# Kernel tuning notes

Hardware: AMD Instinct MI355X
Metric: run time of the kernel (lower is better)

The kernel has to match this reference:

```python
import jax, jax.numpy as jnp
import numpy as np

L = 4          # num_layers
D = 64         # embedding_dim
N = 100000     # nodes
E = 1250000    # edges
B = 2048       # graphs (batch.max()+1, fixed for jit)
ATOM_V = 128   # atom feature vocab per field
BOND_V = 8     # bond feature vocab per field
BN_EPS = 1e-5


def setup_inputs() -> dict:
    key = jax.random.key(0)
    ks = jax.random.split(key, 10)
    x_feat = jax.random.randint(ks[0], (N, 9), 0, 119)
    edge_index = jax.random.randint(ks[1], (2, E), 0, N)
    edge_attr = jax.random.randint(ks[2], (E, 3), 0, 5)
    batch = jnp.sort(jax.random.randint(ks[3], (N,), 0, B))
    s = 0.02
    atom_emb = jax.random.normal(ks[4], (9, ATOM_V, D), jnp.float32) * s
    bond_emb = jax.random.normal(ks[5], (L, 3, BOND_V, D), jnp.float32) * s
    eps = jnp.zeros((L,), jnp.float32)
    W1 = jax.random.normal(ks[6], (L, D, 2 * D), jnp.float32) / np.sqrt(D).astype(np.float32)
    b1 = jnp.zeros((L, 2 * D), jnp.float32)
    bn1_g = jnp.ones((L, 2 * D), jnp.float32)
    bn1_b = jnp.zeros((L, 2 * D), jnp.float32)
    W2 = jax.random.normal(ks[7], (L, 2 * D, D), jnp.float32) / np.sqrt(2 * D).astype(np.float32)
    b2 = jnp.zeros((L, D), jnp.float32)
    bn2_g = jnp.ones((L, D), jnp.float32)
    bn2_b = jnp.zeros((L, D), jnp.float32)
    return dict(atom_emb=atom_emb, bond_emb=bond_emb, eps=eps,
                W1=W1, b1=b1, bn1_g=bn1_g, bn1_b=bn1_b,
                W2=W2, b2=b2, bn2_g=bn2_g, bn2_b=bn2_b,
                x_feat=x_feat, edge_index=edge_index, edge_attr=edge_attr, batch=batch)


def _bn(h, g, b):
    # training-mode BatchNorm1d over node dim (biased variance, as torch forward)
    m = h.mean(axis=0)
    v = jnp.mean((h - m) ** 2, axis=0)
    return (h - m) * jax.lax.rsqrt(v + BN_EPS) * g + b


def reference(atom_emb, bond_emb, eps, W1, b1, bn1_g, bn1_b, W2, b2, bn2_g, bn2_b,
              x_feat, edge_index, edge_attr, batch):
    n = x_feat.shape[0]
    # AtomEncoder: sum of per-field embedding lookups -> [N, D]
    h = atom_emb[jnp.arange(9), x_feat].sum(axis=1)
    src, dst = edge_index[0], edge_index[1]
    for l in range(L):
        # BondEncoder for this layer: [E, D]
        e = bond_emb[l][jnp.arange(3), edge_attr].sum(axis=1)
        # message: relu(x_j + edge_emb); aggregate: scatter_add at target nodes
        msg = jax.nn.relu(h[src] + e)
        agg = jax.ops.segment_sum(msg, dst, num_segments=N)
        z = (1.0 + eps[l]) * h + agg
        # MLP: Linear -> BN -> ReLU -> Linear
        z = jax.nn.relu(_bn(z @ W1[l] + b1[l], bn1_g[l], bn1_b[l]))
        z = z @ W2[l] + b2[l]
        # outer per-layer BatchNorm
        h = _bn(z, bn2_g[l], bn2_b[l])
        if l != L - 1:
            h = jax.nn.relu(h)
        # dropout disabled (eval/deterministic reference)
    node_repr = h
    # mean pooling by graph id
    out_feat = jax.ops.segment_sum(h, batch, num_segments=B)
    cnt = jax.ops.segment_sum(jnp.ones((n, 1), h.dtype), batch, num_segments=B)
    graph_repr = out_feat / (cnt + 1e-9)
    return node_repr, graph_repr
```

## Files before the change

kernel.cpp:

```cpp
#include <hip/hip_runtime.h>

#define NN 100000
#define NE 1250000
#define NB 2048
#define NZB 391

typedef __attribute__((ext_vector_type(8))) short short8;
typedef __attribute__((ext_vector_type(4))) float floatx4;

__device__ inline unsigned short f2bf(float f) {
    unsigned u = __float_as_uint(f);
    u = u + 0x7fffu + ((u >> 16) & 1u);
    return (unsigned short)(u >> 16);
}
__device__ inline float bf2f(unsigned short h) {
    return __uint_as_float(((unsigned)h) << 16);
}

__global__ void atom_encode(const float* __restrict__ atom_emb,
                            const int* __restrict__ x_feat,
                            float* __restrict__ h, unsigned short* __restrict__ h16) {
    int id = blockIdx.x * 256 + threadIdx.x;
    int n = id >> 4, q = id & 15;
    floatx4 acc = {0.f, 0.f, 0.f, 0.f};
    for (int f = 0; f < 9; f++) {
        int v = x_feat[n * 9 + f];
        const floatx4* p = (const floatx4*)(atom_emb + (size_t)(f * 128 + v) * 64);
        acc += p[q];
    }
    ((floatx4*)h)[(size_t)n * 16 + q] = acc;
    ushort4 hv;
    hv.x = f2bf(acc[0]); hv.y = f2bf(acc[1]); hv.z = f2bf(acc[2]); hv.w = f2bf(acc[3]);
    ((ushort4*)h16)[(size_t)n * 16 + q] = hv;
}

__global__ void deg_count(const int* __restrict__ ei, int* __restrict__ csr) {
    int e = (blockIdx.x * 256 + threadIdx.x) * 2;
    if (e < NE) {
        int2 d = *(const int2*)(ei + NE + e);
        atomicAdd(&csr[d.x], 1);
        if (e + 1 < NE) atomicAdd(&csr[d.y], 1);
    }
}

__global__ void scan_local(int* __restrict__ csr, int* __restrict__ bsum) {
    __shared__ int ls[256];
    int tid = threadIdx.x;
    int base = blockIdx.x * 1024 + tid * 4;
    int4 v = make_int4(0, 0, 0, 0);
    if (base + 3 < NN) {
        v = *(const int4*)(csr + base);
    } else {
        if (base + 0 < NN) v.x = csr[base + 0];
        if (base + 1 < NN) v.y = csr[base + 1];
        if (base + 2 < NN) v.z = csr[base + 2];
        if (base + 3 < NN) v.w = csr[base + 3];
    }
    int s = v.x + v.y + v.z + v.w;
    ls[tid] = s;
    __syncthreads();
    for (int d = 1; d < 256; d <<= 1) {
        int t = (tid >= d) ? ls[tid - d] : 0;
        __syncthreads();
        ls[tid] += t;
        __syncthreads();
    }
    if (tid == 255) bsum[blockIdx.x] = ls[255];
    int e0 = tid ? ls[tid - 1] : 0;
    int4 w;
    w.x = e0; w.y = e0 + v.x; w.z = w.y + v.y; w.w = w.z + v.z;
    if (base + 3 < NN) {
        *(int4*)(csr + base) = w;
    } else {
        if (base + 0 < NN) csr[base + 0] = w.x;
        if (base + 1 < NN) csr[base + 1] = w.y;
        if (base + 2 < NN) csr[base + 2] = w.z;
        if (base + 3 < NN) csr[base + 3] = w.w;
    }
}

__global__ void scan_add(int* __restrict__ csr, const int* __restrict__ bsum) {
    __shared__ int red[128];
    int tid = threadIdx.x;
    if (tid < 128) {
        red[tid] = (tid < blockIdx.x && tid < 98) ? bsum[tid] : 0;
    }
    __syncthreads();
    for (int d = 64; d > 0; d >>= 1) {
        if (tid < d) red[tid] += red[tid + d];
        __syncthreads();
    }
    int off = red[0];
    int base = blockIdx.x * 1024 + tid * 4;
    if (base + 3 < NN) {
        int4 v = *(const int4*)(csr + base);
        v.x += off; v.y += off; v.z += off; v.w += off;
        *(int4*)(csr + base) = v;
    } else {
        for (int i = 0; i < 4; i++)
            if (base + i < NN) csr[base + i] += off;
    }
}

__global__ void csr_fill(const int* __restrict__ ei, const int* __restrict__ ea,
                         int* __restrict__ csr, unsigned* __restrict__ epack) {
    int e = blockIdx.x * 256 + threadIdx.x;
    if (e >= NE) return;
    int dst = ei[NE + e];
    unsigned at = (unsigned)(ea[e * 3] | (ea[e * 3 + 1] << 3) | (ea[e * 3 + 2] << 6));
    unsigned rec = (unsigned)ei[e] | (at << 17);
    int pos = atomicAdd(&csr[dst], 1);
    epack[pos] = rec;
}

template <bool HASBN>
__global__ void gather_k(const float* __restrict__ x, const unsigned short* __restrict__ x16,
                         const float* __restrict__ bond_emb,
                         const float* __restrict__ eps, const int* __restrict__ csr,
                         const unsigned* __restrict__ epack, int l,
                         const float* __restrict__ stats, const float* __restrict__ bn_g,
                         const float* __restrict__ bn_b, float* __restrict__ agg) {
    __shared__ float be[24 * 64];
    __shared__ float ca[64], cb[64];
    int tid = threadIdx.x;
    const float* bsrc = bond_emb + (size_t)l * 1536;
    for (int i = tid; i < 1536; i += 256) be[i] = bsrc[i];
    if (tid < 64) {
        if (HASBN) {
            float s = 0.f, ss = 0.f;
            for (int j = 0; j < 8; j++) {
                s  += stats[j * 128 + tid];
                ss += stats[j * 128 + 64 + tid];
            }
            float mean = s / NN;
            float var  = ss / NN - mean * mean;
            float a = bn_g[(l - 1) * 64 + tid] * rsqrtf(var + 1e-5f);
            ca[tid] = a;
            cb[tid] = bn_b[(l - 1) * 64 + tid] - mean * a;
        } else {
            ca[tid] = 1.f; cb[tid] = 0.f;
        }
    }
    __syncthreads();
    int id = blockIdx.x * 256 + tid;
    int n = id >> 4, q = id & 15;
    float s = 1.0f + eps[l];
    floatx4 cav = *(const floatx4*)&ca[q * 4];
    floatx4 cbv = *(const floatx4*)&cb[q * 4];
    floatx4 xv = ((const floatx4*)x)[(size_t)n * 16 + q];
    if (HASBN) {
        xv[0] = fmaxf(cav[0] * xv[0] + cbv[0], 0.f);
        xv[1] = fmaxf(cav[1] * xv[1] + cbv[1], 0.f);
        xv[2] = fmaxf(cav[2] * xv[2] + cbv[2], 0.f);
        xv[3] = fmaxf(cav[3] * xv[3] + cbv[3], 0.f);
    }
    floatx4 acc = xv * s;
    floatx4 accB = {0.f, 0.f, 0.f, 0.f};
    int k0 = n ? csr[n - 1] : 0;
    int k1 = csr[n];
    const floatx4* beq = (const floatx4*)be;
    int k = k0;
    for (; k + 1 < k1; k += 2) {
        unsigned r0 = epack[k];
        unsigned r1 = epack[k + 1];
        ushort4 h0 = ((const ushort4*)x16)[(size_t)(r0 & 0x1FFFFu) * 16 + q];
        ushort4 h1 = ((const ushort4*)x16)[(size_t)(r1 & 0x1FFFFu) * 16 + q];
        floatx4 m0 = {bf2f(h0.x), bf2f(h0.y), bf2f(h0.z), bf2f(h0.w)};
        floatx4 m1 = {bf2f(h1.x), bf2f(h1.y), bf2f(h1.z), bf2f(h1.w)};
        if (HASBN) {
            m0[0] = fmaxf(cav[0] * m0[0] + cbv[0], 0.f);
            m0[1] = fmaxf(cav[1] * m0[1] + cbv[1], 0.f);
            m0[2] = fmaxf(cav[2] * m0[2] + cbv[2], 0.f);
            m0[3] = fmaxf(cav[3] * m0[3] + cbv[3], 0.f);
            m1[0] = fmaxf(cav[0] * m1[0] + cbv[0], 0.f);
            m1[1] = fmaxf(cav[1] * m1[1] + cbv[1], 0.f);
            m1[2] = fmaxf(cav[2] * m1[2] + cbv[2], 0.f);
            m1[3] = fmaxf(cav[3] * m1[3] + cbv[3], 0.f);
        }
        m0 += beq[((r0 >> 17) & 7u) * 16 + q];
        m0 += beq[(8 + ((r0 >> 20) & 7u)) * 16 + q];
        m0 += beq[(16 + ((r0 >> 23) & 7u)) * 16 + q];
        m1 += beq[((r1 >> 17) & 7u) * 16 + q];
        m1 += beq[(8 + ((r1 >> 20) & 7u)) * 16 + q];
        m1 += beq[(16 + ((r1 >> 23) & 7u)) * 16 + q];
        acc[0] += fmaxf(m0[0], 0.f);
        acc[1] += fmaxf(m0[1], 0.f);
        acc[2] += fmaxf(m0[2], 0.f);
        acc[3] += fmaxf(m0[3], 0.f);
        accB[0] += fmaxf(m1[0], 0.f);
        accB[1] += fmaxf(m1[1], 0.f);
        accB[2] += fmaxf(m1[2], 0.f);
        accB[3] += fmaxf(m1[3], 0.f);
    }
    if (k < k1) {
        unsigned r0 = epack[k];
        ushort4 h0 = ((const ushort4*)x16)[(size_t)(r0 & 0x1FFFFu) * 16 + q];
        floatx4 m0 = {bf2f(h0.x), bf2f(h0.y), bf2f(h0.z), bf2f(h0.w)};
        if (HASBN) {
            m0[0] = fmaxf(cav[0] * m0[0] + cbv[0], 0.f);
            m0[1] = fmaxf(cav[1] * m0[1] + cbv[1], 0.f);
            m0[2] = fmaxf(cav[2] * m0[2] + cbv[2], 0.f);
            m0[3] = fmaxf(cav[3] * m0[3] + cbv[3], 0.f);
        }
        m0 += beq[((r0 >> 17) & 7u) * 16 + q];
        m0 += beq[(8 + ((r0 >> 20) & 7u)) * 16 + q];
        m0 += beq[(16 + ((r0 >> 23) & 7u)) * 16 + q];
        acc[0] += fmaxf(m0[0], 0.f);
        acc[1] += fmaxf(m0[1], 0.f);
        acc[2] += fmaxf(m0[2], 0.f);
        acc[3] += fmaxf(m0[3], 0.f);
    }
    acc += accB;
    ((floatx4*)agg)[(size_t)n * 16 + q] = acc;
}

__global__ void wcvt(const float* __restrict__ W1, const float* __restrict__ W2,
                     unsigned short* __restrict__ w1h, unsigned short* __restrict__ w2h) {
    int id = blockIdx.x * 256 + threadIdx.x;
    if (id < 32768) {
        int l = id >> 13, rem = id & 8191, c = rem >> 6, k = rem & 63;
        w1h[id] = f2bf(W1[l * 8192 + k * 128 + c]);
    } else {
        int id2 = id - 32768;
        int l = id2 >> 13, rem = id2 & 8191, c = rem >> 7, k = rem & 127;
        w2h[id2] = f2bf(W2[l * 8192 + k * 64 + c]);
    }
}

#define MFMA __builtin_amdgcn_mfma_f32_16x16x32_bf16

#define ZS 264
__launch_bounds__(256)
__global__ void zstat(const float* __restrict__ z, float* __restrict__ Gpart,
                      float* __restrict__ zsum) {
    __shared__ char smem[67584];
    unsigned short* zh = (unsigned short*)smem;
    unsigned short* zl = zh + 64 * ZS;
    int tid = threadIdx.x;
    int c2 = tid & 31;
    int nof = tid >> 5;
    int wv = tid >> 6, lane = tid & 63, m = lane & 15, qd = lane >> 4;
    float2 csum = make_float2(0.f, 0.f);
    floatx4 acc[8];
    for (int t = 0; t < 8; t++) acc[t] = (floatx4){0.f, 0.f, 0.f, 0.f};
    int base = blockIdx.x * 256;
    for (int it = 0; it < 32; it++) {
        int n = it * 8 + nof;
        int node = base + n;
        float2 v = make_float2(0.f, 0.f);
        if (node < NN) v = ((const float2*)z)[(size_t)node * 32 + c2];
        csum.x += v.x; csum.y += v.y;
        unsigned short hx = f2bf(v.x), hy = f2bf(v.y);
        zh[(2 * c2) * ZS + n] = hx;
        zh[(2 * c2 + 1) * ZS + n] = hy;
        zl[(2 * c2) * ZS + n] = f2bf(v.x - bf2f(hx));
        zl[(2 * c2 + 1) * ZS + n] = f2bf(v.y - bf2f(hy));
    }
    __syncthreads();
    for (int kc = 0; kc < 8; kc++) {
        short8 ah = *(const short8*)&zh[(wv * 16 + m) * ZS + kc * 32 + qd * 8];
        for (int j = 0; j < 4; j++) {
            short8 bh = *(const short8*)&zh[(j * 16 + m) * ZS + kc * 32 + qd * 8];
            short8 bl = *(const short8*)&zl[(j * 16 + m) * ZS + kc * 32 + qd * 8];
            acc[j * 2]     = MFMA(ah, bh, acc[j * 2], 0, 0, 0);
            acc[j * 2 + 1] = MFMA(ah, bl, acc[j * 2 + 1], 0, 0, 0);
        }
    }
    float* gp = Gpart + (size_t)blockIdx.x * 8192;
    for (int j = 0; j < 4; j++)
        for (int r = 0; r < 4; r++) {
            int idx = (wv * 16 + qd * 4 + r) * 64 + j * 16 + m;
            gp[idx] = acc[j * 2][r];
            gp[4096 + idx] = acc[j * 2 + 1][r];
        }
    __syncthreads();
    float* red = (float*)smem;
    red[tid] = csum.x; red[256 + tid] = csum.y;
    __syncthreads();
    if (tid < 32) {
        float sx = 0.f, sy = 0.f;
        for (int k = 0; k < 8; k++) { sx += red[k * 32 + tid]; sy += red[256 + k * 32 + tid]; }
        atomicAdd(&zsum[2 * tid], sx);
        atomicAdd(&zsum[2 * tid + 1], sy);
    }
}

__global__ void greduce(const float* __restrict__ Gpart, float* __restrict__ G) {
    int idx = blockIdx.x * 256 + threadIdx.x;
    int b0 = blockIdx.y * 98;
    int b1 = b0 + 98; if (b1 > NZB) b1 = NZB;
    float s = 0.f;
    for (int b = b0; b < b1; b++) s += Gpart[(size_t)b * 8192 + idx];
    atomicAdd(&G[idx], s);
}

__launch_bounds__(256)
__global__ void bn1stat(const float* __restrict__ W1, const float* __restrict__ b1,
                        const float* __restrict__ G, const float* __restrict__ zsum,
                        int l, const float* __restrict__ bn_g, const float* __restrict__ bn_b,
                        float* __restrict__ cab) {
    __shared__ float wc[64];
    __shared__ float red[256];
    int c = blockIdx.x;
    int tid = threadIdx.x;
    if (tid < 64) wc[tid] = bf2f(f2bf(W1[l * 8192 + tid * 128 + c]));
    __syncthreads();
    float q = 0.f;
    for (int p = 0; p < 16; p++) {
        int idx = p * 256 + tid;
        int i = idx >> 6, j = idx & 63;
        q += wc[i] * wc[j] * (G[idx] + 2.f * G[4096 + idx]);
    }
    red[tid] = q;
    __syncthreads();
    for (int d = 128; d > 0; d >>= 1) {
        if (tid < d) red[tid] += red[tid + d];
        __syncthreads();
    }
    if (tid == 0) {
        float s1 = 0.f;
        for (int k = 0; k < 64; k++) s1 += zsum[k] * wc[k];
        float bc = b1[l * 128 + c];
        double mean = ((double)s1 + (double)NN * (double)bc) / (double)NN;
        double ex2  = ((double)red[0] + 2.0 * (double)bc * (double)s1
                       + (double)NN * (double)bc * (double)bc) / (double)NN;
        float var = (float)(ex2 - mean * mean);
        float a = bn_g[l * 128 + c] * rsqrtf(var + 1e-5f);
        cab[c] = a;
        cab[128 + c] = bn_b[l * 128 + c] - (float)mean * a + a * bc;
    }
}

#define RS 140
__launch_bounds__(256, 4)
__global__ void mlp_fused(const float* __restrict__ z,
                          const unsigned short* __restrict__ w1h,
                          const unsigned short* __restrict__ w2h,
                          const float* __restrict__ b2,
                          const float* __restrict__ cab, int l,
                          float* __restrict__ t2, unsigned short* __restrict__ t216,
                          float* __restrict__ s2f) {
    __shared__ unsigned short smem[4 * 2 * 16 * RS];
    int tid = threadIdx.x;
    int wv = tid >> 6, lane = tid & 63, m = lane & 15, qd = lane >> 4;
    int base = blockIdx.x * 64;
    unsigned short* rbh = smem + wv * (2 * 16 * RS);
    unsigned short* rbl = rbh + 16 * RS;

    int row = base + wv * 16 + m;
    floatx4 z0a = {0.f, 0.f, 0.f, 0.f}, z0b = z0a, z1a = z0a, z1b = z0a;
    if (row < NN) {
        const floatx4* zp = (const floatx4*)z + (size_t)row * 16;
        z0a = zp[qd * 2];
        z0b = zp[qd * 2 + 1];
        z1a = zp[8 + qd * 2];
        z1b = zp[8 + qd * 2 + 1];
    }
    short8 ah0, al0, ah1, al1;
    for (int j = 0; j < 4; j++) {
        unsigned short h;
        h = f2bf(z0a[j]); ah0[j] = (short)h; al0[j] = (short)f2bf(z0a[j] - bf2f(h));
        h = f2bf(z0b[j]); ah0[4 + j] = (short)h; al0[4 + j] = (short)f2bf(z0b[j] - bf2f(h));
        h = f2bf(z1a[j]); ah1[j] = (short)h; al1[j] = (short)f2bf(z1a[j] - bf2f(h));
        h = f2bf(z1b[j]); ah1[4 + j] = (short)h; al1[4 + j] = (short)f2bf(z1b[j] - bf2f(h));
    }

    float caT[8], cbT[8];
    #pragma unroll
    for (int t = 0; t < 8; t++) {
        caT[t] = cab[t * 16 + m];
        cbT[t] = cab[128 + t * 16 + m];
    }

    const unsigned short* w1p = w1h + l * 8192;
    floatx4 acc1[8];
    #pragma unroll
    for (int t = 0; t < 8; t++) {
        const unsigned short* wp = w1p + (t * 16 + m) * 64;
        short8 bh0 = *(const short8*)(wp + qd * 8);
        short8 bh1 = *(const short8*)(wp + 32 + qd * 8);
        floatx4 c0 = {0.f, 0.f, 0.f, 0.f};
        c0 = MFMA(ah0, bh0, c0, 0, 0, 0);
        c0 = MFMA(al0, bh0, c0, 0, 0, 0);
        c0 = MFMA(ah1, bh1, c0, 0, 0, 0);
        c0 = MFMA(al1, bh1, c0, 0, 0, 0);
        acc1[t] = c0;
    }

    #pragma unroll
    for (int t = 0; t < 8; t++) {
        float a = caT[t], b = cbT[t];
        #pragma unroll
        for (int r = 0; r < 4; r++) {
            int rl = qd * 4 + r;
            float rv = fmaxf(a * acc1[t][r] + b, 0.f);
            unsigned short hh = f2bf(rv);
            rbh[rl * RS + t * 16 + m] = hh;
            rbl[rl * RS + t * 16 + m] = f2bf(rv - bf2f(hh));
        }
    }
    short8 ahf[4], alf[4];
    #pragma unroll
    for (int kh = 0; kh < 4; kh++) {
        ahf[kh] = *(const short8*)&rbh[m * RS + kh * 32 + qd * 8];
        alf[kh] = *(const short8*)&rbl[m * RS + kh * 32 + qd * 8];
    }

    const unsigned short* w2p = w2h + l * 8192;
    floatx4 acc2[4];
    #pragma unroll
    for (int t = 0; t < 4; t++) {
        const unsigned short* wp = w2p + (t * 16 + m) * 128;
        floatx4 c0 = {0.f, 0.f, 0.f, 0.f};
        #pragma unroll
        for (int kh = 0; kh < 4; kh++) {
            short8 bh = *(const short8*)(wp + kh * 32 + qd * 8);
            c0 = MFMA(ahf[kh], bh, c0, 0, 0, 0);
            c0 = MFMA(alf[kh], bh, c0, 0, 0, 0);
        }
        acc2[t] = c0;
    }

    float* redw = (float*)rbh;
    const float* bias = b2 + l * 64;
    #pragma unroll
    for (int t = 0; t < 4; t++) {
        int col = t * 16 + m;
        float bv = bias[col];
        float s = 0.f, ss = 0.f;
        #pragma unroll
        for (int r = 0; r < 4; r++) {
            int node = base + wv * 16 + qd * 4 + r;
            if (node < NN) {
                float v = acc2[t][r] + bv;
                t2[(size_t)node * 64 + col] = v;
                t216[(size_t)node * 64 + col] = f2bf(v);
                s += v; ss += v * v;
            }
        }
        redw[col * 4 + qd] = s;
        redw[256 + col * 4 + qd] = ss;
    }
    __syncthreads();
    if (tid < 64) {
        float s = 0.f, ss = 0.f;
        for (int w = 0; w < 4; w++) {
            const float* rw = (const float*)(smem + w * (2 * 16 * RS));
            for (int q = 0; q < 4; q++) {
                s  += rw[tid * 4 + q];
                ss += rw[256 + tid * 4 + q];
            }
        }
        float* dst = s2f + (blockIdx.x & 7) * 128;
        atomicAdd(&dst[tid], s);
        atomicAdd(&dst[64 + tid], ss);
    }
}

__global__ void bnapply_last(const float* __restrict__ t2, const float* __restrict__ bn_g,
                             const float* __restrict__ bn_b, const float* __restrict__ s2f,
                             float* __restrict__ out, float* __restrict__ gsum,
                             float* __restrict__ gcnt, const int* __restrict__ batch) {
    __shared__ float ca[64], cb[64];
    int tid = threadIdx.x;
    if (tid < 64) {
        float s = 0.f, ss = 0.f;
        for (int j = 0; j < 8; j++) {
            s  += s2f[j * 128 + tid];
            ss += s2f[j * 128 + 64 + tid];
        }
        float mean = s / NN;
        float var  = ss / NN - mean * mean;
        float a = bn_g[3 * 64 + tid] * rsqrtf(var + 1e-5f);
        ca[tid] = a;
        cb[tid] = bn_b[3 * 64 + tid] - mean * a;
    }
    __syncthreads();
    int c = tid & 63, nsub = tid >> 6;
    int nodebase = blockIdx.x * 64;
    float accv = 0.f, accc = 0.f;
    int curg = -1;
    for (int it = 0; it < 16; it++) {
        int node = nodebase + it * 4 + nsub;
        if (node < NN) {
            float v = ca[c] * t2[(size_t)node * 64 + c] + cb[c];
            out[(size_t)node * 64 + c] = v;
            int g = batch[node];
            if (g != curg) {
                if (curg >= 0) {
                    atomicAdd(&gsum[(size_t)curg * 64 + c], accv);
                    if (c == 0) atomicAdd(&gcnt[curg], accc);
                }
                curg = g; accv = v; accc = 1.f;
            } else {
                accv += v; accc += 1.f;
            }
        }
    }
    if (curg >= 0) {
        atomicAdd(&gsum[(size_t)curg * 64 + c], accv);
        if (c == 0) atomicAdd(&gcnt[curg], accc);
    }
}

__global__ void pool_div(const float* __restrict__ gsum, const float* __restrict__ gcnt,
                         float* __restrict__ out) {
    int id = blockIdx.x * 256 + threadIdx.x;
    int g = id >> 6;
    out[(size_t)NN * 64 + id] = gsum[id] / (gcnt[g] + 1e-9f);
}

extern "C" void kernel_launch(void* const* d_in, const int* in_sizes, int n_in,
                              void* d_out, int out_size, void* d_ws, size_t ws_size,
                              hipStream_t stream) {
    const float* atom_emb = (const float*)d_in[0];
    const float* bond_emb = (const float*)d_in[1];
    const float* eps      = (const float*)d_in[2];
    const float* W1       = (const float*)d_in[3];
    const float* b1       = (const float*)d_in[4];
    const float* bn1_g    = (const float*)d_in[5];
    const float* bn1_b    = (const float*)d_in[6];
    const float* W2       = (const float*)d_in[7];
    const float* b2       = (const float*)d_in[8];
    const float* bn2_g    = (const float*)d_in[9];
    const float* bn2_b    = (const float*)d_in[10];
    const int* x_feat     = (const int*)d_in[11];
    const int* edge_index = (const int*)d_in[12];
    const int* edge_attr  = (const int*)d_in[13];
    const int* batch      = (const int*)d_in[14];
    float* out = (float*)d_out;

    char* ws = (char*)d_ws;
    float* gsum   = (float*)ws;   ws += (size_t)NB * 64 * 4;
    float* gcnt   = (float*)ws;   ws += NB * 4;
    int* csr      = (int*)ws;     ws += (size_t)NN * 4;
    float* zsum   = (float*)ws;   ws += 4 * 64 * 4;
    float* G      = (float*)ws;   ws += (size_t)4 * 8192 * 4;
    float* s2f    = (float*)ws;   ws += (size_t)4 * 8 * 128 * 4;
    size_t zbytes = (size_t)(ws - (char*)d_ws);
    float* cab      = (float*)ws;     ws += 256 * 4;
    int* bsum       = (int*)ws;       ws += 128 * 4;
    unsigned* epack = (unsigned*)ws;  ws += (size_t)NE * 4;
    float* Gpart = (float*)ws;    ws += (size_t)NZB * 8192 * 4;
    float* xbuf = (float*)ws;     ws += (size_t)NN * 64 * 4;
    unsigned short* x16 = (unsigned short*)ws; ws += (size_t)NN * 64 * 2;
    float* agg  = (float*)ws;     ws += (size_t)NN * 64 * 4;
    unsigned short* w1h = (unsigned short*)ws; ws += 32768 * 2;
    unsigned short* w2h = (unsigned short*)ws; ws += 32768 * 2;

    hipMemsetAsync((void*)gsum, 0, zbytes, stream);

    wcvt<<<256, 256, 0, stream>>>(W1, W2, w1h, w2h);
    deg_count<<<2442, 256, 0, stream>>>(edge_index, csr);
    scan_local<<<98, 256, 0, stream>>>(csr, bsum);
    scan_add<<<98, 256, 0, stream>>>(csr, bsum);
    csr_fill<<<4883, 256, 0, stream>>>(edge_index, edge_attr, csr, epack);
    atom_encode<<<6250, 256, 0, stream>>>(atom_emb, x_feat, xbuf, x16);

    for (int l = 0; l < 4; l++) {
        if (l == 0) {
            gather_k<false><<<6250, 256, 0, stream>>>(xbuf, x16, bond_emb, eps, csr, epack, l,
                                                      nullptr, nullptr, nullptr, agg);
        } else {
            gather_k<true><<<6250, 256, 0, stream>>>(xbuf, x16, bond_emb, eps, csr, epack, l,
                                                     s2f + (size_t)(l - 1) * 1024,
                                                     bn2_g, bn2_b, agg);
        }
        float* Gl = G + (size_t)l * 8192;
        zstat<<<NZB, 256, 0, stream>>>(agg, Gpart, zsum + l * 64);
        greduce<<<dim3(32, 4), 256, 0, stream>>>(Gpart, Gl);
        bn1stat<<<128, 256, 0, stream>>>(W1, b1, Gl, zsum + l * 64, l, bn1_g, bn1_b, cab);
        mlp_fused<<<1563, 256, 0, stream>>>(agg, w1h, w2h, b2, cab, l,
                                            xbuf, x16, s2f + (size_t)l * 1024);
    }
    bnapply_last<<<1563, 256, 0, stream>>>(xbuf, bn2_g, bn2_b, s2f + (size_t)3 * 1024,
                                           out, gsum, gcnt, batch);
    pool_div<<<512, 256, 0, stream>>>(gsum, gcnt, out);
}
```

Measured before the change: 890.5 us.

## Shard edges by destination range into per-XCC FIFOs before CSR build

Replaces the direct degree-count and CSR-fill passes with a staging pass that bins edges into 64 FIFOs, keyed by destination shard and block id. Two follow-up passes then drain those FIFOs, preferring queues matched to the XCC they run on. The aim is to keep atomics on csr local to one XCD's L2 and so cut cross-die atomic traffic. In exchange it adds an extra pass that writes and reads about 10 MB, a fixed FIFO capacity (FCAP) that could overflow on skewed inputs, and extra atomics for work stealing.

```diff
diff --git a/kernel.cpp b/kernel.cpp
--- a/kernel.cpp
+++ b/kernel.cpp
@@ -4,6 +4,7 @@
 #define NE 1250000
 #define NB 2048
 #define NZB 391
+#define FCAP 21504
 
 typedef __attribute__((ext_vector_type(8))) short short8;
 typedef __attribute__((ext_vector_type(4))) float floatx4;
@@ -15,6 +16,12 @@
 }
 __device__ inline float bf2f(unsigned short h) {
     return __uint_as_float(((unsigned)h) << 16);
+}
+
+__device__ inline int xcc8() {
+    int x;
+    asm volatile("s_getreg_b32 %0, hwreg(HW_REG_XCC_ID, 0, 32)" : "=s"(x));
+    return x & 7;
 }
 
 __global__ void atom_encode(const float* __restrict__ atom_emb,
@@ -34,12 +41,60 @@
     ((ushort4*)h16)[(size_t)n * 16 + q] = hv;
 }
 
-__global__ void deg_count(const int* __restrict__ ei, int* __restrict__ csr) {
-    int e = (blockIdx.x * 256 + threadIdx.x) * 2;
-    if (e < NE) {
-        int2 d = *(const int2*)(ei + NE + e);
-        atomicAdd(&csr[d.x], 1);
-        if (e + 1 < NE) atomicAdd(&csr[d.y], 1);
+__global__ void stage_edges(const int* __restrict__ ei, const int* __restrict__ ea,
+                            int* __restrict__ fcnt, unsigned long long* __restrict__ fifo) {
+    int lane = threadIdx.x & 63;
+    int bmod = blockIdx.x & 7;
+    for (int e = blockIdx.x * 256 + threadIdx.x; e < NE; e += 1024 * 256) {
+        int src = ei[e];
+        int dst = ei[NE + e];
+        unsigned at = (unsigned)(ea[e * 3] | (ea[e * 3 + 1] << 3) | (ea[e * 3 + 2] << 6));
+        unsigned long long v = ((unsigned long long)(unsigned)dst << 32)
+                             | (unsigned)src | (at << 17);
+        int shard = dst / 12500;
+        #pragma unroll
+        for (int s = 0; s < 8; s++) {
+            unsigned long long mask = __ballot(shard == s);
+            if (mask == 0) continue;
+            int leader = __builtin_ctzll(mask);
+            int base;
+            if (lane == leader) base = atomicAdd(&fcnt[(s * 8 + bmod) * 16], __popcll(mask));
+            base = __shfl(base, leader);
+            if (shard == s) {
+                int off = __popcll(mask & ((1ull << lane) - 1));
+                fifo[(size_t)(s * 8 + bmod) * FCAP + base + off] = v;
+            }
+        }
+    }
+}
+
+template <bool FILL>
+__global__ void fifo_pass(const unsigned long long* __restrict__ fifo,
+                          const int* __restrict__ fcnt, int* __restrict__ wq,
+                          int* __restrict__ csr, unsigned* __restrict__ epack) {
+    int lane = threadIdx.x & 63;
+    int myx = xcc8();
+    for (int r = 0; r < 64; r++) {
+        int q = (myx * 8 + r) & 63;
+        int n = fcnt[q * 16];
+        const unsigned long long* f = fifo + (size_t)q * FCAP;
+        while (true) {
+            int base;
+            if (lane == 0) base = atomicAdd(&wq[q * 16], 1024);
+            base = __shfl(base, 0);
+            if (base >= n) break;
+            int end = base + 1024; if (end > n) end = n;
+            for (int i = base + lane; i < end; i += 64) {
+                unsigned long long v = f[i];
+                int dst = (int)(v >> 32);
+                if (FILL) {
+                    int pos = atomicAdd(&csr[dst], 1);
+                    epack[pos] = (unsigned)v;
+                } else {
+                    atomicAdd(&csr[dst], 1);
+                }
+            }
+        }
     }
 }
 
@@ -100,17 +155,6 @@
         for (int i = 0; i < 4; i++)
             if (base + i < NN) csr[base + i] += off;
     }
-}
-
-__global__ void csr_fill(const int* __restrict__ ei, const int* __restrict__ ea,
-                         int* __restrict__ csr, unsigned* __restrict__ epack) {
-    int e = blockIdx.x * 256 + threadIdx.x;
-    if (e >= NE) return;
-    int dst = ei[NE + e];
-    unsigned at = (unsigned)(ea[e * 3] | (ea[e * 3 + 1] << 3) | (ea[e * 3 + 2] << 6));
-    unsigned rec = (unsigned)ei[e] | (at << 17);
-    int pos = atomicAdd(&csr[dst], 1);
-    epack[pos] = rec;
 }
 
 template <bool HASBN>
@@ -537,6 +581,9 @@
     float* zsum   = (float*)ws;   ws += 4 * 64 * 4;
     float* G      = (float*)ws;   ws += (size_t)4 * 8192 * 4;
     float* s2f    = (float*)ws;   ws += (size_t)4 * 8 * 128 * 4;
+    int* fcnt     = (int*)ws;     ws += 64 * 16 * 4;
+    int* wqB      = (int*)ws;     ws += 64 * 16 * 4;
+    int* wqC      = (int*)ws;     ws += 64 * 16 * 4;
     size_t zbytes = (size_t)(ws - (char*)d_ws);
     float* cab      = (float*)ws;     ws += 256 * 4;
     int* bsum       = (int*)ws;       ws += 128 * 4;
@@ -547,14 +594,16 @@
     float* agg  = (float*)ws;     ws += (size_t)NN * 64 * 4;
     unsigned short* w1h = (unsigned short*)ws; ws += 32768 * 2;
     unsigned short* w2h = (unsigned short*)ws; ws += 32768 * 2;
+    unsigned long long* fifo = (unsigned long long*)ws; ws += (size_t)64 * FCAP * 8;
 
     hipMemsetAsync((void*)gsum, 0, zbytes, stream);
 
     wcvt<<<256, 256, 0, stream>>>(W1, W2, w1h, w2h);
-    deg_count<<<2442, 256, 0, stream>>>(edge_index, csr);
+    stage_edges<<<1024, 256, 0, stream>>>(edge_index, edge_attr, fcnt, fifo);
+    fifo_pass<false><<<512, 256, 0, stream>>>(fifo, fcnt, wqB, csr, nullptr);
     scan_local<<<98, 256, 0, stream>>>(csr, bsum);
     scan_add<<<98, 256, 0, stream>>>(csr, bsum);
-    csr_fill<<<4883, 256, 0, stream>>>(edge_index, edge_attr, csr, epack);
+    fifo_pass<true><<<512, 256, 0, stream>>>(fifo, fcnt, wqC, csr, epack);
     atom_encode<<<6250, 256, 0, stream>>>(atom_emb, x_feat, xbuf, x16);
 
     for (int l = 0; l < 4; l++) {
```

After: 1.052 ms. +18.1%, slower.

## Build CSR via two-pass bucket sort instead of global atomics and scans

Applied to the files above, without the earlier changes.

Replaces the degree-count, two-kernel scan, and atomic scatter fill with a two-pass bucket sort. The first pass bins edges into 196 destination buckets of 512 nodes each, using shared-memory staging. The second pass performs a per-bucket local counting sort in shared memory to produce the CSR offsets and the packed edge records. This cuts four launches to two and moves scattered global atomics into LDS, at the cost of an 8-byte-per-edge intermediate buffer with a fixed per-bucket capacity (7168) that could overflow on skewed inputs.

```diff
diff --git a/kernel.cpp b/kernel.cpp
--- a/kernel.cpp
+++ b/kernel.cpp
@@ -4,6 +4,9 @@
 #define NE 1250000
 #define NB 2048
 #define NZB 391
+#define NBK 196
+#define BCAP 7168
+#define ARND 2048
 
 typedef __attribute__((ext_vector_type(8))) short short8;
 typedef __attribute__((ext_vector_type(4))) float floatx4;
@@ -34,83 +37,122 @@
     ((ushort4*)h16)[(size_t)n * 16 + q] = hv;
 }
 
-__global__ void deg_count(const int* __restrict__ ei, int* __restrict__ csr) {
-    int e = (blockIdx.x * 256 + threadIdx.x) * 2;
-    if (e < NE) {
-        int2 d = *(const int2*)(ei + NE + e);
-        atomicAdd(&csr[d.x], 1);
-        if (e + 1 < NE) atomicAdd(&csr[d.y], 1);
-    }
-}
-
-__global__ void scan_local(int* __restrict__ csr, int* __restrict__ bsum) {
-    __shared__ int ls[256];
+
+__launch_bounds__(256)
+__global__ void bucketA(const int* __restrict__ ei, const int* __restrict__ ea,
+                        int* __restrict__ bcnt, unsigned long long* __restrict__ bbuf) {
+    __shared__ int cnt[256], inc[256], cur[256], gpos[256];
+    __shared__ unsigned long long buf[ARND];
+    __shared__ unsigned short bos[ARND];
     int tid = threadIdx.x;
-    int base = blockIdx.x * 1024 + tid * 4;
-    int4 v = make_int4(0, 0, 0, 0);
-    if (base + 3 < NN) {
-        v = *(const int4*)(csr + base);
-    } else {
-        if (base + 0 < NN) v.x = csr[base + 0];
-        if (base + 1 < NN) v.y = csr[base + 1];
-        if (base + 2 < NN) v.z = csr[base + 2];
-        if (base + 3 < NN) v.w = csr[base + 3];
-    }
-    int s = v.x + v.y + v.z + v.w;
-    ls[tid] = s;
+    cnt[tid] = 0; cur[tid] = 0;
+    __syncthreads();
+    int base = blockIdx.x * ARND;
+    unsigned long long rec[8]; int bb[8];
+    #pragma unroll
+    for (int i = 0; i < 8; i++) {
+        int e = base + i * 256 + tid;
+        if (e < NE) {
+            int src = ei[e];
+            int dst = ei[NE + e];
+            unsigned at = (unsigned)(ea[e * 3] | (ea[e * 3 + 1] << 3) | (ea[e * 3 + 2] << 6));
+            rec[i] = ((unsigned long long)(unsigned)dst << 32)
+                   | (unsigned)src | (at << 17);
+            bb[i] = dst >> 9;
+            atomicAdd(&cnt[bb[i]], 1);
+        } else bb[i] = -1;
+    }
+    __syncthreads();
+    int v = cnt[tid];
+    inc[tid] = v;
     __syncthreads();
     for (int d = 1; d < 256; d <<= 1) {
-        int t = (tid >= d) ? ls[tid - d] : 0;
-        __syncthreads();
-        ls[tid] += t;
-        __syncthreads();
-    }
-    if (tid == 255) bsum[blockIdx.x] = ls[255];
-    int e0 = tid ? ls[tid - 1] : 0;
-    int4 w;
-    w.x = e0; w.y = e0 + v.x; w.z = w.y + v.y; w.w = w.z + v.z;
-    if (base + 3 < NN) {
-        *(int4*)(csr + base) = w;
-    } else {
-        if (base + 0 < NN) csr[base + 0] = w.x;
-        if (base + 1 < NN) csr[base + 1] = w.y;
-        if (base + 2 < NN) csr[base + 2] = w.z;
-        if (base + 3 < NN) csr[base + 3] = w.w;
-    }
-}
-
-__global__ void scan_add(int* __restrict__ csr, const int* __restrict__ bsum) {
-    __shared__ int red[128];
+        int t = (tid >= d) ? inc[tid - d] : 0;
+        __syncthreads();
+        inc[tid] += t;
+        __syncthreads();
+    }
+    if (v > 0) gpos[tid] = atomicAdd(&bcnt[tid], v);
+    __syncthreads();
+    #pragma unroll
+    for (int i = 0; i < 8; i++) {
+        if (bb[i] >= 0) {
+            int b = bb[i];
+            int p = atomicAdd(&cur[b], 1);
+            int slot = (inc[b] - cnt[b]) + p;
+            buf[slot] = rec[i];
+            bos[slot] = (unsigned short)b;
+        }
+    }
+    __syncthreads();
+    int nval = inc[255];
+    for (int s = tid; s < nval; s += 256) {
+        int b = bos[s];
+        int off = s - (inc[b] - cnt[b]);
+        bbuf[(size_t)b * BCAP + gpos[b] + off] = buf[s];
+    }
+}
+
+__launch_bounds__(256)
+__global__ void bucketB(const int* __restrict__ bcnt,
+                        const unsigned long long* __restrict__ bbuf,
+                        int* __restrict__ csr, unsigned* __restrict__ epack) {
+    __shared__ int c[512], cs[512], s[256], bp[256], sh[1];
     int tid = threadIdx.x;
-    if (tid < 128) {
-        red[tid] = (tid < blockIdx.x && tid < 98) ? bsum[tid] : 0;
-    }
-    __syncthreads();
-    for (int d = 64; d > 0; d >>= 1) {
-        if (tid < d) red[tid] += red[tid + d];
-        __syncthreads();
-    }
-    int off = red[0];
-    int base = blockIdx.x * 1024 + tid * 4;
-    if (base + 3 < NN) {
-        int4 v = *(const int4*)(csr + base);
-        v.x += off; v.y += off; v.z += off; v.w += off;
-        *(int4*)(csr + base) = v;
-    } else {
-        for (int i = 0; i < 4; i++)
-            if (base + i < NN) csr[base + i] += off;
-    }
-}
-
-__global__ void csr_fill(const int* __restrict__ ei, const int* __restrict__ ea,
-                         int* __restrict__ csr, unsigned* __restrict__ epack) {
-    int e = blockIdx.x * 256 + threadIdx.x;
-    if (e >= NE) return;
-    int dst = ei[NE + e];
-    unsigned at = (unsigned)(ea[e * 3] | (ea[e * 3 + 1] << 3) | (ea[e * 3 + 2] << 6));
-    unsigned rec = (unsigned)ei[e] | (at << 17);
-    int pos = atomicAdd(&csr[dst], 1);
-    epack[pos] = rec;
+    int b = blockIdx.x;
+    bp[tid] = (tid < NBK) ? bcnt[tid] : 0;
+    c[tid] = 0; c[256 + tid] = 0;
+    __syncthreads();
+    for (int d = 1; d < 256; d <<= 1) {
+        int t = (tid >= d) ? bp[tid - d] : 0;
+        __syncthreads();
+        bp[tid] += t;
+        __syncthreads();
+    }
+    int gbase = b ? bp[b - 1] : 0;
+    int cnt = bcnt[b];
+    const unsigned long long* f = bbuf + (size_t)b * BCAP;
+    int n0 = b << 9;
+    for (int i = tid; i < cnt; i += 256) {
+        int idx = (int)(f[i] >> 32) - n0;
+        atomicAdd(&c[idx], 1);
+    }
+    __syncthreads();
+    cs[tid] = c[tid]; cs[256 + tid] = c[256 + tid];
+    s[tid] = c[tid];
+    __syncthreads();
+    for (int d = 1; d < 256; d <<= 1) {
+        int t = (tid >= d) ? s[tid - d] : 0;
+        __syncthreads();
+        s[tid] += t;
+        __syncthreads();
+    }
+    c[tid] = s[tid];
+    if (tid == 255) sh[0] = s[255];
+    __syncthreads();
+    s[tid] = c[256 + tid];
+    __syncthreads();
+    for (int d = 1; d < 256; d <<= 1) {
+        int t = (tid >= d) ? s[tid - d] : 0;
+        __syncthreads();
+        s[tid] += t;
+        __syncthreads();
+    }
+    c[256 + tid] = s[tid] + sh[0];
+    __syncthreads();
+    int nn = NN - n0; if (nn > 512) nn = 512;
+    for (int i = tid; i < 512; i += 256) {
+        int start = gbase + c[i] - cs[i];
+        if (i < nn) csr[n0 + i] = gbase + c[i];
+        cs[i] = start;
+    }
+    __syncthreads();
+    for (int i = tid; i < cnt; i += 256) {
+        unsigned long long v = f[i];
+        int idx = (int)(v >> 32) - n0;
+        int p = atomicAdd(&cs[idx], 1);
+        epack[p] = (unsigned)v;
+    }
 }
 
 template <bool HASBN>
@@ -533,13 +575,13 @@
     char* ws = (char*)d_ws;
     float* gsum   = (float*)ws;   ws += (size_t)NB * 64 * 4;
     float* gcnt   = (float*)ws;   ws += NB * 4;
-    int* csr      = (int*)ws;     ws += (size_t)NN * 4;
     float* zsum   = (float*)ws;   ws += 4 * 64 * 4;
     float* G      = (float*)ws;   ws += (size_t)4 * 8192 * 4;
     float* s2f    = (float*)ws;   ws += (size_t)4 * 8 * 128 * 4;
+    int* bcnt     = (int*)ws;     ws += 256 * 4;
     size_t zbytes = (size_t)(ws - (char*)d_ws);
+    int* csr        = (int*)ws;       ws += (size_t)NN * 4;
     float* cab      = (float*)ws;     ws += 256 * 4;
-    int* bsum       = (int*)ws;       ws += 128 * 4;
     unsigned* epack = (unsigned*)ws;  ws += (size_t)NE * 4;
     float* Gpart = (float*)ws;    ws += (size_t)NZB * 8192 * 4;
     float* xbuf = (float*)ws;     ws += (size_t)NN * 64 * 4;
@@ -547,14 +589,13 @@
     float* agg  = (float*)ws;     ws += (size_t)NN * 64 * 4;
     unsigned short* w1h = (unsigned short*)ws; ws += 32768 * 2;
     unsigned short* w2h = (unsigned short*)ws; ws += 32768 * 2;
+    unsigned long long* bbuf = (unsigned long long*)ws; ws += (size_t)NBK * BCAP * 8;
 
     hipMemsetAsync((void*)gsum, 0, zbytes, stream);
 
     wcvt<<<256, 256, 0, stream>>>(W1, W2, w1h, w2h);
-    deg_count<<<2442, 256, 0, stream>>>(edge_index, csr);
-    scan_local<<<98, 256, 0, stream>>>(csr, bsum);
-    scan_add<<<98, 256, 0, stream>>>(csr, bsum);
-    csr_fill<<<4883, 256, 0, stream>>>(edge_index, edge_attr, csr, epack);
+    bucketA<<<(NE + ARND - 1) / ARND, 256, 0, stream>>>(edge_index, edge_attr, bcnt, bbuf);
+    bucketB<<<NBK, 256, 0, stream>>>(bcnt, bbuf, csr, epack);
     atom_encode<<<6250, 256, 0, stream>>>(atom_emb, x_feat, xbuf, x16);
 
     for (int l = 0; l < 4; l++) {
```

Result: faster. 821.8 us (-7.7%).
